# Optimization experiments

Measured on AMD Instinct MI355X. Metric: run time of the kernel, lower is better.

The kernel has to match this reference:

```python
import jax, jax.numpy as jnp
import numpy as np

F = 32  # node channels (both convs)


def ecc_conv(x, src, dst, e, fgn_w, fgn_b, root, bias):
    """Edge-conditioned conv: per-edge kernel from edge feats, gather-matmul-scatter."""
    n_nodes = x.shape[0]
    n_edges = e.shape[0]
    f_in = x.shape[1]
    # filter-generating network: (E, S) -> (E, F_in*F_out) -> (E, F_in, F_out)
    kernels = (e @ fgn_w + fgn_b).reshape(n_edges, f_in, F)
    # gather source node feats, per-edge matmul
    messages = jnp.einsum('ef,efo->eo', x[src], kernels)
    # scatter-sum to target nodes
    agg = jax.ops.segment_sum(messages, dst, num_segments=n_nodes)
    return jax.nn.relu(agg + x @ root + bias)


def setup_inputs() -> dict:
    key = jax.random.key(0)
    ks = jax.random.split(key, 12)
    N, E, S = 50000, 200000, 16
    s = 0.05  # small init scale to keep activations bounded through relu
    return {
        'x': jax.random.normal(ks[0], (N, F), jnp.float32),
        'e': jax.random.normal(ks[1], (E, S), jnp.float32),
        'src': jax.random.randint(ks[2], (E,), 0, N, jnp.int32),
        'dst': jax.random.randint(ks[3], (E,), 0, N, jnp.int32),
        'fgn_w1': jax.random.normal(ks[4], (S, F * F), jnp.float32) * s,
        'fgn_b1': jnp.zeros((F * F,), jnp.float32),
        'root1': jax.random.normal(ks[5], (F, F), jnp.float32) * s,
        'bias1': jnp.zeros((F,), jnp.float32),
        'fgn_w2': jax.random.normal(ks[6], (S, F * F), jnp.float32) * s,
        'fgn_b2': jnp.zeros((F * F,), jnp.float32),
        'root2': jax.random.normal(ks[7], (F, F), jnp.float32) * s,
        'bias2': jnp.zeros((F,), jnp.float32),
        'dense_w': jax.random.normal(ks[8], (F, 1), jnp.float32) * s,
        'dense_b': jnp.zeros((1,), jnp.float32),
    }


def reference(x, e, src, dst, fgn_w1, fgn_b1, root1, bias1,
              fgn_w2, fgn_b2, root2, bias2, dense_w, dense_b):
    h = ecc_conv(x, src, dst, e, fgn_w1, fgn_b1, root1, bias1)
    h = ecc_conv(h, src, dst, e, fgn_w2, fgn_b2, root2, bias2)
    pooled = jnp.sum(h, axis=0)          # global sum pool over nodes -> (F,)
    return pooled @ dense_w + dense_b    # (1,)
```

## Files before the change

kernel.cpp:

```cpp
#include <hip/hip_runtime.h>
#include <hip/hip_bf16.h>
#include <hip/hip_fp16.h>

#define F 32
#define S 16

typedef short v8s __attribute__((ext_vector_type(8)));
typedef _Float16 v8h __attribute__((ext_vector_type(8)));
typedef float v4f __attribute__((ext_vector_type(4)));

__device__ __forceinline__ float bf_lo(unsigned u) { return __uint_as_float(u << 16); }
__device__ __forceinline__ float bf_hi(unsigned u) { return __uint_as_float(u & 0xffff0000u); }
__device__ __forceinline__ unsigned short f2bf(float f) {
    __hip_bfloat16 h = __float2bfloat16(f);
    return *(unsigned short*)&h;
}
__device__ __forceinline__ unsigned short f2h(float f) {
    __half h = __float2half(f);
    return *(unsigned short*)&h;
}
__device__ __forceinline__ unsigned pack2(float a, float b) {
    __hip_bfloat162 h2 = __float22bfloat162_rn(make_float2(a, b));
    return *(unsigned*)&h2;
}
static inline size_t align256(size_t b) { return (b + 255) & ~(size_t)255; }

__global__ __launch_bounds__(256) void prep_kernel(
    const float* __restrict__ w1, const float* __restrict__ b1, const float* __restrict__ r1,
    const float* __restrict__ w2, const float* __restrict__ b2, const float* __restrict__ r2,
    unsigned short* __restrict__ Wf1, unsigned short* __restrict__ Wf2,
    unsigned short* __restrict__ Rt1, unsigned short* __restrict__ Rt2,
    const int* __restrict__ dst, int* __restrict__ cnt, int E)
{
    const int PER = 34 * 512 + 32 * 32;
    if (blockIdx.x < 144) {
        int tid = blockIdx.x * blockDim.x + threadIdx.x;
        if (tid >= 2 * PER) return;
        const int layer = tid / PER;
        const int rem   = tid % PER;
        const float* w = layer ? w2 : w1;
        const float* b = layer ? b2 : b1;
        const float* r = layer ? r2 : r1;
        if (rem < 34 * 512) {
            const int fi   = rem >> 9;
            const int rr   = rem & 511;
            const int lane = rr >> 3;
            const int j    = rr & 7;
            const int half = fi & 1;
            const int ck   = fi >> 1;
            const int o    = (half << 4) | (lane & 15);
            const int k    = ck * 32 + (lane >> 4) * 8 + j;
            const int s    = k >> 5, f = k & 31;
            const float v  = (s < S) ? w[s * (F * F) + f * F + o] : b[f * F + o];
            (layer ? Wf2 : Wf1)[rem] = f2h(v);
        } else {
            const int q = rem - 34 * 512;
            const int o = q >> 5, f = q & 31;
            (layer ? Rt2 : Rt1)[o * F + f] = f2bf(r[f * F + o]);
        }
    } else {
        const int e = (blockIdx.x - 144) * blockDim.x + threadIdx.x;
        if (e < E) atomicAdd(&cnt[dst[e]], 1);
    }
}

__global__ __launch_bounds__(256) void scan_partial(
    const int* __restrict__ cnt, int* __restrict__ partial, int N)
{
    const int i = blockIdx.x * 256 + threadIdx.x;
    int v = (i < N) ? cnt[i] : 0;
    #pragma unroll
    for (int off = 32; off > 0; off >>= 1) v += __shfl_down(v, off, 64);
    __shared__ int wsum[4];
    const int wave = threadIdx.x >> 6, lane = threadIdx.x & 63;
    if (lane == 0) wsum[wave] = v;
    __syncthreads();
    if (threadIdx.x == 0)
        partial[blockIdx.x] = wsum[0] + wsum[1] + wsum[2] + wsum[3];
}

__global__ void scan_top(int* __restrict__ partial, int M)
{
    const int t = threadIdx.x;
    int carry = 0;
    for (int base = 0; base < M; base += 64) {
        const int i = base + t;
        const int v0 = (i < M) ? partial[i] : 0;
        int v = v0;
        #pragma unroll
        for (int off = 1; off < 64; off <<= 1) {
            int u = __shfl_up(v, off, 64);
            if (t >= off) v += u;
        }
        if (i < M) partial[i] = carry + (v - v0);
        carry += __shfl(v, 63, 64);
    }
}

__global__ __launch_bounds__(256) void scan_final(
    const int* __restrict__ cnt, const int* __restrict__ partial,
    int* __restrict__ cursor, int* __restrict__ rowptr, int N)
{
    const int i = blockIdx.x * 256 + threadIdx.x;
    const int v0 = (i < N) ? cnt[i] : 0;
    int v = v0;
    const int wave = threadIdx.x >> 6, lane = threadIdx.x & 63;
    #pragma unroll
    for (int off = 1; off < 64; off <<= 1) {
        int u = __shfl_up(v, off, 64);
        if (lane >= off) v += u;
    }
    __shared__ int wsum[4];
    if (lane == 63) wsum[wave] = v;
    __syncthreads();
    int woff = 0;
    for (int ww = 0; ww < 4; ++ww) woff += (ww < wave) ? wsum[ww] : 0;
    if (i < N) {
        const int excl = partial[blockIdx.x] + woff + (v - v0);
        cursor[i] = excl;
        rowptr[i] = excl;
    }
}

__global__ __launch_bounds__(256) void scatter_kernel(
    const int* __restrict__ dst, int* __restrict__ cursor,
    int* __restrict__ perm, int E)
{
    int e = blockIdx.x * blockDim.x + threadIdx.x;
    if (e < E) {
        int p = atomicAdd(&cursor[dst[e]], 1);
        perm[p] = e;
    }
}

__global__ __launch_bounds__(256) void edge_msg(
    const float* __restrict__ xin,
    const float* __restrict__ ef,
    const int* __restrict__ src,
    const unsigned short* __restrict__ Wf,
    unsigned short* __restrict__ msg,
    int E)
{
    __shared__ v8h Wl[34 * 64];
    const int tid  = threadIdx.x;
    const int w    = tid >> 6;
    const int lane = tid & 63;
    const int lid  = lane & 15;
    const int quad = lane >> 4;

    {
        const uint4* s = (const uint4*)Wf;
        uint4* d = (uint4*)Wl;
        #pragma unroll
        for (int i = 0; i < 9; ++i) {
            const int idx = tid + 256 * i;
            if (idx < 2176) d[idx] = s[idx];
        }
    }
    __syncthreads();

    const int nTiles = (E + 15) >> 4;
    const int stride = gridDim.x * 4;
    int tile = blockIdx.x * 4 + w;
    if (tile >= nTiles) return;

    int  slot = tile * 16 + lid;
    bool live = (slot < E);
    int  s0   = live ? slot : 0;
    int  sn   = src[s0];
    const float4* xp = (const float4*)(xin + (size_t)sn * F + quad * 8);
    float4 xv0 = xp[0], xv1 = xp[1];
    const float4* efv = (const float4*)(ef + (size_t)s0 * S);
    float4 c0 = efv[0], c1 = efv[1], c2 = efv[2], c3 = efv[3];

    while (true) {
        const int nextTile = tile + stride;
        float4 nxv0, nxv1, nc0, nc1, nc2, nc3;
        bool nlive = false;
        if (nextTile < nTiles) {
            const int  ns_  = nextTile * 16 + lid;
            nlive = (ns_ < E);
            const int  ns0_ = nlive ? ns_ : 0;
            const int  nsn  = src[ns0_];
            const float4* nxp = (const float4*)(xin + (size_t)nsn * F + quad * 8);
            nxv0 = nxp[0]; nxv1 = nxp[1];
            const float4* nefv = (const float4*)(ef + (size_t)ns0_ * S);
            nc0 = nefv[0]; nc1 = nefv[1]; nc2 = nefv[2]; nc3 = nefv[3];
        }

        const float cs[S] = {c0.x, c0.y, c0.z, c0.w, c1.x, c1.y, c1.z, c1.w,
                             c2.x, c2.y, c2.z, c2.w, c3.x, c3.y, c3.z, c3.w};

        union { v8h h8; __half2 h2[4]; } xh;
        xh.h2[0] = __floats2half2_rn(xv0.x, xv0.y);
        xh.h2[1] = __floats2half2_rn(xv0.z, xv0.w);
        xh.h2[2] = __floats2half2_rn(xv1.x, xv1.y);
        xh.h2[3] = __floats2half2_rn(xv1.z, xv1.w);

        v4f acc0 = {0.f, 0.f, 0.f, 0.f};
        v4f acc1 = {0.f, 0.f, 0.f, 0.f};

        #pragma unroll
        for (int ck = 0; ck < S; ++ck) {
            const __half2 c2 = __floats2half2_rn(cs[ck], cs[ck]);
            union { v8h h8; __half2 h2[4]; } fr;
            fr.h2[0] = __hmul2(c2, xh.h2[0]);
            fr.h2[1] = __hmul2(c2, xh.h2[1]);
            fr.h2[2] = __hmul2(c2, xh.h2[2]);
            fr.h2[3] = __hmul2(c2, xh.h2[3]);
            acc0 = __builtin_amdgcn_mfma_f32_16x16x32_f16(Wl[(2 * ck) * 64 + lane],     fr.h8, acc0, 0, 0, 0);
            acc1 = __builtin_amdgcn_mfma_f32_16x16x32_f16(Wl[(2 * ck + 1) * 64 + lane], fr.h8, acc1, 0, 0, 0);
        }
        acc0 = __builtin_amdgcn_mfma_f32_16x16x32_f16(Wl[32 * 64 + lane], xh.h8, acc0, 0, 0, 0);
        acc1 = __builtin_amdgcn_mfma_f32_16x16x32_f16(Wl[33 * 64 + lane], xh.h8, acc1, 0, 0, 0);

        if (live) {
            unsigned short* mp = msg + (size_t)slot * 32;
            uint2 p0, p1;
            p0.x = pack2(acc0[0], acc0[1]);
            p0.y = pack2(acc0[2], acc0[3]);
            p1.x = pack2(acc1[0], acc1[1]);
            p1.y = pack2(acc1[2], acc1[3]);
            *(uint2*)(mp + quad * 4)      = p0;
            *(uint2*)(mp + 16 + quad * 4) = p1;
        }

        if (nextTile >= nTiles) break;
        tile = nextTile;
        slot = tile * 16 + lid;
        live = nlive;
        xv0 = nxv0; xv1 = nxv1;
        c0 = nc0; c1 = nc1; c2 = nc2; c3 = nc3;
    }
}

__global__ __launch_bounds__(256) void rootsum(
    const float* __restrict__ in,
    const unsigned short* __restrict__ msg,
    const int* __restrict__ rowptr,
    const int* __restrict__ cnt,
    const int* __restrict__ perm,
    const unsigned short* __restrict__ Rt,
    const float* __restrict__ bias,
    float* __restrict__ h,
    int N)
{
    __shared__ float acc[64 * 33];
    __shared__ unsigned short As[64 * F];
    const int tid  = threadIdx.x;
    const int n0   = blockIdx.x * 64;
    const int w    = tid >> 6;
    const int lane = tid & 63;
    const int lid  = lane & 15;
    const int quad = lane >> 4;

    {
        const int nl = tid >> 2;
        const int kq = tid & 3;
        int n = n0 + nl; if (n > N - 1) n = N - 1;
        const float4* xp = (const float4*)(in + (size_t)n * F + kq * 8);
        float4 v0 = xp[0], v1 = xp[1];
        uint4 pk;
        pk.x = pack2(v0.x, v0.y);
        pk.y = pack2(v0.z, v0.w);
        pk.z = pack2(v1.x, v1.y);
        pk.w = pack2(v1.z, v1.w);
        const int slot = ((nl >> 4) * 4 + kq) * 16 + (nl & 15);
        *(uint4*)(As + slot * 8) = pk;
    }

    {
        const int nl = tid >> 2;
        const int oq = tid & 3;
        const int n  = n0 + nl;
        float a[8];
        #pragma unroll
        for (int j = 0; j < 8; ++j) a[j] = 0.f;
        if (n < N) {
            const int k0 = rowptr[n];
            const int k1 = k0 + cnt[n];
            for (int k = k0; k < k1; ++k) {
                const int e = perm[k];
                const uint4 q = *(const uint4*)(msg + (size_t)e * 32 + oq * 8);
                a[0] += bf_lo(q.x); a[1] += bf_hi(q.x);
                a[2] += bf_lo(q.y); a[3] += bf_hi(q.y);
                a[4] += bf_lo(q.z); a[5] += bf_hi(q.z);
                a[6] += bf_lo(q.w); a[7] += bf_hi(q.w);
            }
        }
        float* ap = acc + nl * 33 + oq * 8;
        #pragma unroll
        for (int j = 0; j < 8; ++j) ap[j] = a[j];
    }
    __syncthreads();

    const int jt  = w & 1;
    const int ns0 = (w >> 1) * 2;
    const v8s rf = *(const v8s*)(Rt + (size_t)(jt * 16 + lid) * F + quad * 8);
    const int o0 = jt * 16 + quad * 4;
    const float4 bs = *(const float4*)(bias + o0);

    #pragma unroll
    for (int i = 0; i < 2; ++i) {
        const int ns = ns0 + i;
        const v8s af = *(const v8s*)(As + (((ns * 4 + quad) * 16) + lid) * 8);
        v4f d = {0.f, 0.f, 0.f, 0.f};
        d = __builtin_amdgcn_mfma_f32_16x16x32_bf16(rf, af, d, 0, 0, 0);
        const int n = n0 + ns * 16 + lid;
        if (n < N) {
            const float* ap = acc + (ns * 16 + lid) * 33 + o0;
            float4 hv;
            hv.x = fmaxf(d[0] + ap[0] + bs.x, 0.f);
            hv.y = fmaxf(d[1] + ap[1] + bs.y, 0.f);
            hv.z = fmaxf(d[2] + ap[2] + bs.z, 0.f);
            hv.w = fmaxf(d[3] + ap[3] + bs.w, 0.f);
            *(float4*)(h + (size_t)n * F + o0) = hv;
        }
    }
}

__global__ __launch_bounds__(256) void rootsum_pool(
    const float* __restrict__ in,
    const unsigned short* __restrict__ msg,
    const int* __restrict__ rowptr,
    const int* __restrict__ cnt,
    const int* __restrict__ perm,
    const unsigned short* __restrict__ Rt,
    const float* __restrict__ bias,
    float* __restrict__ bs,
    int N)
{
    __shared__ float acc[64 * 33];
    __shared__ unsigned short As[64 * F];
    __shared__ float poolbuf[4][16];
    const int tid  = threadIdx.x;
    const int n0   = blockIdx.x * 64;
    const int w    = tid >> 6;
    const int lane = tid & 63;
    const int lid  = lane & 15;
    const int quad = lane >> 4;

    {
        const int nl = tid >> 2;
        const int kq = tid & 3;
        int n = n0 + nl; if (n > N - 1) n = N - 1;
        const float4* xp = (const float4*)(in + (size_t)n * F + kq * 8);
        float4 v0 = xp[0], v1 = xp[1];
        uint4 pk;
        pk.x = pack2(v0.x, v0.y);
        pk.y = pack2(v0.z, v0.w);
        pk.z = pack2(v1.x, v1.y);
        pk.w = pack2(v1.z, v1.w);
        const int slot = ((nl >> 4) * 4 + kq) * 16 + (nl & 15);
        *(uint4*)(As + slot * 8) = pk;
    }

    {
        const int nl = tid >> 2;
        const int oq = tid & 3;
        const int n  = n0 + nl;
        float a[8];
        #pragma unroll
        for (int j = 0; j < 8; ++j) a[j] = 0.f;
        if (n < N) {
            const int k0 = rowptr[n];
            const int k1 = k0 + cnt[n];
            for (int k = k0; k < k1; ++k) {
                const int e = perm[k];
                const uint4 q = *(const uint4*)(msg + (size_t)e * 32 + oq * 8);
                a[0] += bf_lo(q.x); a[1] += bf_hi(q.x);
                a[2] += bf_lo(q.y); a[3] += bf_hi(q.y);
                a[4] += bf_lo(q.z); a[5] += bf_hi(q.z);
                a[6] += bf_lo(q.w); a[7] += bf_hi(q.w);
            }
        }
        float* ap = acc + nl * 33 + oq * 8;
        #pragma unroll
        for (int j = 0; j < 8; ++j) ap[j] = a[j];
    }
    __syncthreads();

    const int jt  = w & 1;
    const int ns0 = (w >> 1) * 2;
    const v8s rf = *(const v8s*)(Rt + (size_t)(jt * 16 + lid) * F + quad * 8);
    const int o0 = jt * 16 + quad * 4;
    const float4 bs4 = *(const float4*)(bias + o0);

    float psum[4] = {0.f, 0.f, 0.f, 0.f};

    #pragma unroll
    for (int i = 0; i < 2; ++i) {
        const int ns = ns0 + i;
        const v8s af = *(const v8s*)(As + (((ns * 4 + quad) * 16) + lid) * 8);
        v4f d = {0.f, 0.f, 0.f, 0.f};
        d = __builtin_amdgcn_mfma_f32_16x16x32_bf16(rf, af, d, 0, 0, 0);
        const int n = n0 + ns * 16 + lid;
        if (n < N) {
            const float* ap = acc + (ns * 16 + lid) * 33 + o0;
            psum[0] += fmaxf(d[0] + ap[0] + bs4.x, 0.f);
            psum[1] += fmaxf(d[1] + ap[1] + bs4.y, 0.f);
            psum[2] += fmaxf(d[2] + ap[2] + bs4.z, 0.f);
            psum[3] += fmaxf(d[3] + ap[3] + bs4.w, 0.f);
        }
    }

    #pragma unroll
    for (int m = 1; m < 16; m <<= 1) {
        psum[0] += __shfl_xor(psum[0], m, 64);
        psum[1] += __shfl_xor(psum[1], m, 64);
        psum[2] += __shfl_xor(psum[2], m, 64);
        psum[3] += __shfl_xor(psum[3], m, 64);
    }
    if (lid == 0) {
        #pragma unroll
        for (int j = 0; j < 4; ++j) poolbuf[w][quad * 4 + j] = psum[j];
    }
    __syncthreads();
    if (tid < 32) {
        const int jt2 = tid >> 4, idx = tid & 15;
        bs[(size_t)blockIdx.x * 32 + tid] = poolbuf[jt2][idx] + poolbuf[jt2 + 2][idx];
    }
}

__global__ __launch_bounds__(256) void final_fused(
    const float* __restrict__ bs, int nb,
    const float* __restrict__ dw, const float* __restrict__ db,
    float* __restrict__ out)
{
    const int ch = threadIdx.x & 31, g = threadIdx.x >> 5;
    float s = 0.f;
    for (int b = g; b < nb; b += 8) s += bs[(size_t)b * 32 + ch];
    __shared__ float red[256];
    red[threadIdx.x] = s;
    __syncthreads();
    if (threadIdx.x < 128) red[threadIdx.x] += red[threadIdx.x + 128];
    __syncthreads();
    if (threadIdx.x < 64) red[threadIdx.x] += red[threadIdx.x + 64];
    __syncthreads();
    if (threadIdx.x < 32) red[threadIdx.x] = (red[threadIdx.x] + red[threadIdx.x + 32]) * dw[threadIdx.x];
    __syncthreads();
    if (threadIdx.x == 0) {
        float t = 0.f;
        #pragma unroll
        for (int i = 0; i < 32; ++i) t += red[i];
        out[0] = t + db[0];
    }
}

__global__ __launch_bounds__(256) void pool_kernel(
    const float* __restrict__ h, float* __restrict__ pooled, int N)
{
    const int c = threadIdx.x & (F - 1);
    float p = 0.0f;
    for (int n = blockIdx.x * 8 + (threadIdx.x >> 5); n < N; n += gridDim.x * 8)
        p += h[(size_t)n * F + c];
    __shared__ float red[256];
    red[threadIdx.x] = p;
    __syncthreads();
    for (int off = 128; off >= F; off >>= 1) {
        if (threadIdx.x < off) red[threadIdx.x] += red[threadIdx.x + off];
        __syncthreads();
    }
    if (threadIdx.x < F) atomicAdd(&pooled[threadIdx.x], red[threadIdx.x]);
}

__global__ void final_kernel(
    const float* __restrict__ pooled, const float* __restrict__ dw,
    const float* __restrict__ db, float* __restrict__ out)
{
    const int o = threadIdx.x;
    float v = (o < F) ? pooled[o] * dw[o] : 0.0f;
    #pragma unroll
    for (int off = 32; off > 0; off >>= 1) v += __shfl_down(v, off, 64);
    if (o == 0) out[0] = v + db[0];
}

__global__ __launch_bounds__(256, 2) void ecc_edge_slow(
    const float* __restrict__ x, const float* __restrict__ ef,
    const int* __restrict__ src, const int* __restrict__ dst,
    const float* __restrict__ W, const float* __restrict__ B,
    float* __restrict__ agg, int E)
{
    const int tid = blockIdx.x * blockDim.x + threadIdx.x;
    const bool live = (tid < E);
    const int e = live ? tid : (E - 1);
    const int sn = src[e], dn = dst[e];
    float xr[F];
    const float4* xp = (const float4*)(x + (size_t)sn * F);
    #pragma unroll
    for (int i = 0; i < F / 4; ++i) {
        float4 v = xp[i];
        xr[4*i+0] = v.x; xr[4*i+1] = v.y; xr[4*i+2] = v.z; xr[4*i+3] = v.w;
    }
    float acc[F];
    #pragma unroll
    for (int o = 0; o < F; ++o) acc[o] = 0.0f;
    const float* erow = ef + (size_t)e * S;
    for (int s = 0; s < S; ++s) {
        const float es = erow[s];
        const float* Ws = W + s * (F * F);
        #pragma unroll
        for (int f = 0; f < F; ++f) {
            const float z = es * xr[f];
            #pragma unroll
            for (int o = 0; o < F; ++o) acc[o] = fmaf(z, Ws[f * F + o], acc[o]);
        }
    }
    #pragma unroll
    for (int f = 0; f < F; ++f) {
        const float xf = xr[f];
        #pragma unroll
        for (int o = 0; o < F; ++o) acc[o] = fmaf(xf, B[f * F + o], acc[o]);
    }
    if (live) {
        float* ap = agg + (size_t)dn * F;
        #pragma unroll
        for (int o = 0; o < F; ++o) atomicAdd(ap + o, acc[o]);
    }
}

__global__ __launch_bounds__(256) void ecc_node_slow(
    const float* __restrict__ xin, const float* __restrict__ root,
    const float* __restrict__ bias, float* __restrict__ h, int N)
{
    int t = blockIdx.x * blockDim.x + threadIdx.x;
    if (t >= N * F) return;
    const int n = t >> 5, o = t & (F - 1);
    const float* xrow = xin + (size_t)n * F;
    float v = h[t] + bias[o];
    #pragma unroll
    for (int f = 0; f < F; ++f) v = fmaf(xrow[f], root[f * F + o], v);
    h[t] = fmaxf(v, 0.0f);
}

extern "C" void kernel_launch(void* const* d_in, const int* in_sizes, int n_in,
                              void* d_out, int out_size, void* d_ws, size_t ws_size,
                              hipStream_t stream) {
    const float* x      = (const float*)d_in[0];
    const float* efeat  = (const float*)d_in[1];
    const int*   src    = (const int*)d_in[2];
    const int*   dst    = (const int*)d_in[3];
    const float* fgn_w1 = (const float*)d_in[4];
    const float* fgn_b1 = (const float*)d_in[5];
    const float* root1  = (const float*)d_in[6];
    const float* bias1  = (const float*)d_in[7];
    const float* fgn_w2 = (const float*)d_in[8];
    const float* fgn_b2 = (const float*)d_in[9];
    const float* root2  = (const float*)d_in[10];
    const float* bias2  = (const float*)d_in[11];
    const float* dense_w = (const float*)d_in[12];
    const float* dense_b = (const float*)d_in[13];

    const int N = in_sizes[0] / F;
    const int E = in_sizes[2];

    const int gridP    = (N + 255) / 256;
    const int rsBlocks = (N + 63) / 64;

    const size_t pooledB = 256;
    const size_t cntB    = align256((size_t)N * 4);
    const size_t rowB    = align256((size_t)N * 4);
    const size_t curB    = align256((size_t)N * 4);
    const size_t partB   = align256((size_t)gridP * 4);
    const size_t permB   = align256((size_t)E * 4);
    const size_t efsB    = align256((size_t)E * S * 4);
    const size_t srcsB   = align256((size_t)E * 4);
    const size_t msgB    = align256((size_t)E * 32 * 2);
    const size_t hB      = (size_t)N * F * 4;
    const size_t wfB     = align256((size_t)34 * 512 * 2);
    const size_t rtB     = align256((size_t)32 * 32 * 2);

    const size_t offCnt  = pooledB;
    const size_t offRow  = offCnt + cntB;
    const size_t offCur  = offRow + rowB;
    const size_t offPart = offCur + curB;
    const size_t offPerm = offPart + partB;
    const size_t offEfs  = offPerm + permB;
    const size_t offSrcs = offEfs + efsB;
    const size_t offMsg  = offSrcs + srcsB;
    const size_t offH1   = offMsg + msgB;
    const size_t offH2   = offH1 + hB;
    const size_t offW1   = offH2 + hB;
    const size_t offW2   = offW1 + wfB;
    const size_t offR1   = offW2 + wfB;
    const size_t offR2   = offR1 + rtB;
    const size_t need    = offR2 + rtB;

    const int eB         = (E + 255) / 256;
    const int nodeBlocks = (N * F + 255) / 256;

    if (ws_size >= need) {
        int* cnt     = (int*)((char*)d_ws + offCnt);
        int* rowptr  = (int*)((char*)d_ws + offRow);
        int* cursor  = (int*)((char*)d_ws + offCur);
        int* partial = (int*)((char*)d_ws + offPart);
        int* perm    = (int*)((char*)d_ws + offPerm);
        unsigned short* msg = (unsigned short*)((char*)d_ws + offMsg);
        float* h1    = (float*)((char*)d_ws + offH1);
        float* bsum  = (float*)((char*)d_ws + offH2);
        unsigned short* Wf1 = (unsigned short*)((char*)d_ws + offW1);
        unsigned short* Wf2 = (unsigned short*)((char*)d_ws + offW2);
        unsigned short* Rt1 = (unsigned short*)((char*)d_ws + offR1);
        unsigned short* Rt2 = (unsigned short*)((char*)d_ws + offR2);

        hipMemsetAsync((char*)d_ws + offCnt, 0, cntB, stream);

        prep_kernel<<<144 + eB, 256, 0, stream>>>(
            fgn_w1, fgn_b1, root1, fgn_w2, fgn_b2, root2,
            Wf1, Wf2, Rt1, Rt2, dst, cnt, E);

        scan_partial  <<<gridP, 256, 0, stream>>>(cnt, partial, N);
        scan_top      <<<1, 64, 0, stream>>>(partial, gridP);
        scan_final    <<<gridP, 256, 0, stream>>>(cnt, partial, cursor, rowptr, N);
        scatter_kernel<<<eB, 256, 0, stream>>>(dst, cursor, perm, E);

        const int nTiles = (E + 15) / 16;
        int edgeBlocks = (nTiles + 3) / 4;
        if (edgeBlocks > 1024) edgeBlocks = 1024;

        edge_msg<<<edgeBlocks, 256, 0, stream>>>(x, efeat, src, Wf1, msg, E);
        rootsum <<<rsBlocks, 256, 0, stream>>>(x, msg, rowptr, cnt, perm, Rt1, bias1, h1, N);

        edge_msg    <<<edgeBlocks, 256, 0, stream>>>(h1, efeat, src, Wf2, msg, E);
        rootsum_pool<<<rsBlocks, 256, 0, stream>>>(h1, msg, rowptr, cnt, perm, Rt2, bias2, bsum, N);

        final_fused<<<1, 256, 0, stream>>>(bsum, rsBlocks, dense_w, dense_b, (float*)d_out);
    } else {
        float* agg1   = (float*)d_ws;
        float* agg2   = agg1 + (size_t)N * F;
        float* pooled = agg2 + (size_t)N * F;
        hipMemsetAsync(d_ws, 0, (2 * (size_t)N * F + F) * sizeof(float), stream);
        ecc_edge_slow<<<eB, 256, 0, stream>>>(x, efeat, src, dst, fgn_w1, fgn_b1, agg1, E);
        ecc_node_slow<<<nodeBlocks, 256, 0, stream>>>(x, root1, bias1, agg1, N);
        ecc_edge_slow<<<eB, 256, 0, stream>>>(agg1, efeat, src, dst, fgn_w2, fgn_b2, agg2, E);
        ecc_node_slow<<<nodeBlocks, 256, 0, stream>>>(agg1, root2, bias2, agg2, N);
        pool_kernel <<<512, 256, 0, stream>>>(agg2, pooled, N);
        final_kernel<<<1, 64, 0, stream>>>(pooled, dense_w, dense_b, (float*)d_out);
    }
}
```

Baseline: 200.0 us.

## Store node features as fp16, fuse scan top-level and final reduction into neighbors

Converts the input node features to fp16 in the prep kernel and writes layer-1 output in fp16, so the edge gather and the second rootsum read half the bytes. The single-block scan_top launch is removed: each scan_final block now sums its preceding partials itself. The final pooled reduction kernel is folded into rootsum_pool with a last-block-done atomic counter. This cuts gather bandwidth and two launches, at the cost of extra fp16 rounding on the layer-1 activations and redundant partial summation in scan_final.

```diff
diff --git a/kernel.cpp b/kernel.cpp
--- a/kernel.cpp
+++ b/kernel.cpp
@@ -23,6 +23,10 @@
     __hip_bfloat162 h2 = __float22bfloat162_rn(make_float2(a, b));
     return *(unsigned*)&h2;
 }
+__device__ __forceinline__ unsigned pack2h(float a, float b) {
+    __half2 h2 = __floats2half2_rn(a, b);
+    return *(unsigned*)&h2;
+}
 static inline size_t align256(size_t b) { return (b + 255) & ~(size_t)255; }
 
 __global__ __launch_bounds__(256) void prep_kernel(
@@ -30,7 +34,9 @@
     const float* __restrict__ w2, const float* __restrict__ b2, const float* __restrict__ r2,
     unsigned short* __restrict__ Wf1, unsigned short* __restrict__ Wf2,
     unsigned short* __restrict__ Rt1, unsigned short* __restrict__ Rt2,
-    const int* __restrict__ dst, int* __restrict__ cnt, int E)
+    const int* __restrict__ dst, int* __restrict__ cnt,
+    const float* __restrict__ x, unsigned short* __restrict__ x16,
+    int N, int E, int eB)
 {
     const int PER = 34 * 512 + 32 * 32;
     if (blockIdx.x < 144) {
@@ -58,9 +64,19 @@
             const int o = q >> 5, f = q & 31;
             (layer ? Rt2 : Rt1)[o * F + f] = f2bf(r[f * F + o]);
         }
-    } else {
+    } else if (blockIdx.x < 144 + eB) {
         const int e = (blockIdx.x - 144) * blockDim.x + threadIdx.x;
         if (e < E) atomicAdd(&cnt[dst[e]], 1);
+    } else {
+        const int idx = (blockIdx.x - 144 - eB) * 256 + threadIdx.x;
+        if (idx < N * 4) {
+            const float4* p = (const float4*)(x + (size_t)idx * 8);
+            float4 a = p[0], b = p[1];
+            uint4 o;
+            o.x = pack2h(a.x, a.y); o.y = pack2h(a.z, a.w);
+            o.z = pack2h(b.x, b.y); o.w = pack2h(b.z, b.w);
+            *(uint4*)(x16 + (size_t)idx * 8) = o;
+        }
     }
 }
 
@@ -79,32 +95,27 @@
         partial[blockIdx.x] = wsum[0] + wsum[1] + wsum[2] + wsum[3];
 }
 
-__global__ void scan_top(int* __restrict__ partial, int M)
-{
-    const int t = threadIdx.x;
-    int carry = 0;
-    for (int base = 0; base < M; base += 64) {
-        const int i = base + t;
-        const int v0 = (i < M) ? partial[i] : 0;
-        int v = v0;
-        #pragma unroll
-        for (int off = 1; off < 64; off <<= 1) {
-            int u = __shfl_up(v, off, 64);
-            if (t >= off) v += u;
-        }
-        if (i < M) partial[i] = carry + (v - v0);
-        carry += __shfl(v, 63, 64);
-    }
-}
-
 __global__ __launch_bounds__(256) void scan_final(
     const int* __restrict__ cnt, const int* __restrict__ partial,
     int* __restrict__ cursor, int* __restrict__ rowptr, int N)
 {
-    const int i = blockIdx.x * 256 + threadIdx.x;
+    const int tid = threadIdx.x;
+    __shared__ int pacc[256];
+    int pre = 0;
+    for (int j = tid; j < blockIdx.x; j += 256) pre += partial[j];
+    pacc[tid] = pre;
+    __syncthreads();
+    #pragma unroll
+    for (int off = 128; off > 0; off >>= 1) {
+        if (tid < off) pacc[tid] += pacc[tid + off];
+        __syncthreads();
+    }
+    const int blockPre = pacc[0];
+
+    const int i = blockIdx.x * 256 + tid;
     const int v0 = (i < N) ? cnt[i] : 0;
     int v = v0;
-    const int wave = threadIdx.x >> 6, lane = threadIdx.x & 63;
+    const int wave = tid >> 6, lane = tid & 63;
     #pragma unroll
     for (int off = 1; off < 64; off <<= 1) {
         int u = __shfl_up(v, off, 64);
@@ -116,7 +127,7 @@
     int woff = 0;
     for (int ww = 0; ww < 4; ++ww) woff += (ww < wave) ? wsum[ww] : 0;
     if (i < N) {
-        const int excl = partial[blockIdx.x] + woff + (v - v0);
+        const int excl = blockPre + woff + (v - v0);
         cursor[i] = excl;
         rowptr[i] = excl;
     }
@@ -134,7 +145,7 @@
 }
 
 __global__ __launch_bounds__(256) void edge_msg(
-    const float* __restrict__ xin,
+    const unsigned short* __restrict__ x16,
     const float* __restrict__ ef,
     const int* __restrict__ src,
     const unsigned short* __restrict__ Wf,
@@ -168,22 +179,21 @@
     bool live = (slot < E);
     int  s0   = live ? slot : 0;
     int  sn   = src[s0];
-    const float4* xp = (const float4*)(xin + (size_t)sn * F + quad * 8);
-    float4 xv0 = xp[0], xv1 = xp[1];
+    v8h xh = *(const v8h*)(x16 + (size_t)sn * F + quad * 8);
     const float4* efv = (const float4*)(ef + (size_t)s0 * S);
     float4 c0 = efv[0], c1 = efv[1], c2 = efv[2], c3 = efv[3];
 
     while (true) {
         const int nextTile = tile + stride;
-        float4 nxv0, nxv1, nc0, nc1, nc2, nc3;
+        v8h nxh;
+        float4 nc0, nc1, nc2, nc3;
         bool nlive = false;
         if (nextTile < nTiles) {
             const int  ns_  = nextTile * 16 + lid;
             nlive = (ns_ < E);
             const int  ns0_ = nlive ? ns_ : 0;
             const int  nsn  = src[ns0_];
-            const float4* nxp = (const float4*)(xin + (size_t)nsn * F + quad * 8);
-            nxv0 = nxp[0]; nxv1 = nxp[1];
+            nxh = *(const v8h*)(x16 + (size_t)nsn * F + quad * 8);
             const float4* nefv = (const float4*)(ef + (size_t)ns0_ * S);
             nc0 = nefv[0]; nc1 = nefv[1]; nc2 = nefv[2]; nc3 = nefv[3];
         }
@@ -191,28 +201,25 @@
         const float cs[S] = {c0.x, c0.y, c0.z, c0.w, c1.x, c1.y, c1.z, c1.w,
                              c2.x, c2.y, c2.z, c2.w, c3.x, c3.y, c3.z, c3.w};
 
-        union { v8h h8; __half2 h2[4]; } xh;
-        xh.h2[0] = __floats2half2_rn(xv0.x, xv0.y);
-        xh.h2[1] = __floats2half2_rn(xv0.z, xv0.w);
-        xh.h2[2] = __floats2half2_rn(xv1.x, xv1.y);
-        xh.h2[3] = __floats2half2_rn(xv1.z, xv1.w);
+        union { v8h h8; __half2 h2[4]; } xu;
+        xu.h8 = xh;
 
         v4f acc0 = {0.f, 0.f, 0.f, 0.f};
         v4f acc1 = {0.f, 0.f, 0.f, 0.f};
 
         #pragma unroll
         for (int ck = 0; ck < S; ++ck) {
-            const __half2 c2 = __floats2half2_rn(cs[ck], cs[ck]);
+            const __half2 cc = __floats2half2_rn(cs[ck], cs[ck]);
             union { v8h h8; __half2 h2[4]; } fr;
-            fr.h2[0] = __hmul2(c2, xh.h2[0]);
-            fr.h2[1] = __hmul2(c2, xh.h2[1]);
-            fr.h2[2] = __hmul2(c2, xh.h2[2]);
-            fr.h2[3] = __hmul2(c2, xh.h2[3]);
+            fr.h2[0] = __hmul2(cc, xu.h2[0]);
+            fr.h2[1] = __hmul2(cc, xu.h2[1]);
+            fr.h2[2] = __hmul2(cc, xu.h2[2]);
+            fr.h2[3] = __hmul2(cc, xu.h2[3]);
             acc0 = __builtin_amdgcn_mfma_f32_16x16x32_f16(Wl[(2 * ck) * 64 + lane],     fr.h8, acc0, 0, 0, 0);
             acc1 = __builtin_amdgcn_mfma_f32_16x16x32_f16(Wl[(2 * ck + 1) * 64 + lane], fr.h8, acc1, 0, 0, 0);
         }
-        acc0 = __builtin_amdgcn_mfma_f32_16x16x32_f16(Wl[32 * 64 + lane], xh.h8, acc0, 0, 0, 0);
-        acc1 = __builtin_amdgcn_mfma_f32_16x16x32_f16(Wl[33 * 64 + lane], xh.h8, acc1, 0, 0, 0);
+        acc0 = __builtin_amdgcn_mfma_f32_16x16x32_f16(Wl[32 * 64 + lane], xu.h8, acc0, 0, 0, 0);
+        acc1 = __builtin_amdgcn_mfma_f32_16x16x32_f16(Wl[33 * 64 + lane], xu.h8, acc1, 0, 0, 0);
 
         if (live) {
             unsigned short* mp = msg + (size_t)slot * 32;
@@ -229,7 +236,7 @@
         tile = nextTile;
         slot = tile * 16 + lid;
         live = nlive;
-        xv0 = nxv0; xv1 = nxv1;
+        xh = nxh;
         c0 = nc0; c1 = nc1; c2 = nc2; c3 = nc3;
     }
 }
@@ -242,7 +249,7 @@
     const int* __restrict__ perm,
     const unsigned short* __restrict__ Rt,
     const float* __restrict__ bias,
-    float* __restrict__ h,
+    unsigned short* __restrict__ h16,
     int N)
 {
     __shared__ float acc[64 * 33];
@@ -314,13 +321,16 @@
             hv.y = fmaxf(d[1] + ap[1] + bs.y, 0.f);
             hv.z = fmaxf(d[2] + ap[2] + bs.z, 0.f);
             hv.w = fmaxf(d[3] + ap[3] + bs.w, 0.f);
-            *(float4*)(h + (size_t)n * F + o0) = hv;
+            uint2 hp;
+            hp.x = pack2h(hv.x, hv.y);
+            hp.y = pack2h(hv.z, hv.w);
+            *(uint2*)(h16 + (size_t)n * F + o0) = hp;
         }
     }
 }
 
 __global__ __launch_bounds__(256) void rootsum_pool(
-    const float* __restrict__ in,
+    const unsigned short* __restrict__ in16,
     const unsigned short* __restrict__ msg,
     const int* __restrict__ rowptr,
     const int* __restrict__ cnt,
@@ -328,6 +338,10 @@
     const unsigned short* __restrict__ Rt,
     const float* __restrict__ bias,
     float* __restrict__ bs,
+    int* __restrict__ flag,
+    const float* __restrict__ dw,
+    const float* __restrict__ db,
+    float* __restrict__ out,
     int N)
 {
     __shared__ float acc[64 * 33];
@@ -344,13 +358,17 @@
         const int nl = tid >> 2;
         const int kq = tid & 3;
         int n = n0 + nl; if (n > N - 1) n = N - 1;
-        const float4* xp = (const float4*)(in + (size_t)n * F + kq * 8);
-        float4 v0 = xp[0], v1 = xp[1];
+        const uint4 hv4 = *(const uint4*)(in16 + (size_t)n * F + kq * 8);
+        const __half2* hh = (const __half2*)&hv4;
+        float2 f0 = __half22float2(hh[0]);
+        float2 f1 = __half22float2(hh[1]);
+        float2 f2 = __half22float2(hh[2]);
+        float2 f3 = __half22float2(hh[3]);
         uint4 pk;
-        pk.x = pack2(v0.x, v0.y);
-        pk.y = pack2(v0.z, v0.w);
-        pk.z = pack2(v1.x, v1.y);
-        pk.w = pack2(v1.z, v1.w);
+        pk.x = pack2(f0.x, f0.y);
+        pk.y = pack2(f1.x, f1.y);
+        pk.z = pack2(f2.x, f2.y);
+        pk.w = pack2(f3.x, f3.y);
         const int slot = ((nl >> 4) * 4 + kq) * 16 + (nl & 15);
         *(uint4*)(As + slot * 8) = pk;
     }
@@ -420,30 +438,35 @@
         const int jt2 = tid >> 4, idx = tid & 15;
         bs[(size_t)blockIdx.x * 32 + tid] = poolbuf[jt2][idx] + poolbuf[jt2 + 2][idx];
     }
-}
-
-__global__ __launch_bounds__(256) void final_fused(
-    const float* __restrict__ bs, int nb,
-    const float* __restrict__ dw, const float* __restrict__ db,
-    float* __restrict__ out)
-{
-    const int ch = threadIdx.x & 31, g = threadIdx.x >> 5;
-    float s = 0.f;
-    for (int b = g; b < nb; b += 8) s += bs[(size_t)b * 32 + ch];
-    __shared__ float red[256];
-    red[threadIdx.x] = s;
-    __syncthreads();
-    if (threadIdx.x < 128) red[threadIdx.x] += red[threadIdx.x + 128];
-    __syncthreads();
-    if (threadIdx.x < 64) red[threadIdx.x] += red[threadIdx.x + 64];
-    __syncthreads();
-    if (threadIdx.x < 32) red[threadIdx.x] = (red[threadIdx.x] + red[threadIdx.x + 32]) * dw[threadIdx.x];
-    __syncthreads();
-    if (threadIdx.x == 0) {
-        float t = 0.f;
-        #pragma unroll
-        for (int i = 0; i < 32; ++i) t += red[i];
-        out[0] = t + db[0];
+
+    __shared__ int amLast;
+    __threadfence();
+    if (tid == 0) {
+        const int prev = atomicAdd(flag, 1);
+        amLast = (prev == (int)gridDim.x - 1);
+    }
+    __syncthreads();
+    if (amLast) {
+        __threadfence();
+        const int ch = tid & 31, g = tid >> 5;
+        float s = 0.f;
+        const int nb = gridDim.x;
+        for (int b = g; b < nb; b += 8) s += bs[(size_t)b * 32 + ch];
+        __shared__ float red[256];
+        red[tid] = s;
+        __syncthreads();
+        if (tid < 128) red[tid] += red[tid + 128];
+        __syncthreads();
+        if (tid < 64) red[tid] += red[tid + 64];
+        __syncthreads();
+        if (tid < 32) red[tid] = (red[tid] + red[tid + 32]) * dw[tid];
+        __syncthreads();
+        if (tid == 0) {
+            float t = 0.f;
+            #pragma unroll
+            for (int i = 0; i < 32; ++i) t += red[i];
+            out[0] = t + db[0];
+        }
     }
 }
 
@@ -569,6 +592,7 @@
     const size_t hB      = (size_t)N * F * 4;
     const size_t wfB     = align256((size_t)34 * 512 * 2);
     const size_t rtB     = align256((size_t)32 * 32 * 2);
+    const size_t x16B    = align256((size_t)N * F * 2);
 
     const size_t offCnt  = pooledB;
     const size_t offRow  = offCnt + cntB;
@@ -589,28 +613,30 @@
     const int eB         = (E + 255) / 256;
     const int nodeBlocks = (N * F + 255) / 256;
 
-    if (ws_size >= need) {
+    if (ws_size >= need && efsB >= 2 * x16B) {
+        int* flag    = (int*)d_ws;
         int* cnt     = (int*)((char*)d_ws + offCnt);
         int* rowptr  = (int*)((char*)d_ws + offRow);
         int* cursor  = (int*)((char*)d_ws + offCur);
         int* partial = (int*)((char*)d_ws + offPart);
         int* perm    = (int*)((char*)d_ws + offPerm);
+        unsigned short* x16 = (unsigned short*)((char*)d_ws + offEfs);
+        unsigned short* h16 = (unsigned short*)((char*)d_ws + offEfs + x16B);
         unsigned short* msg = (unsigned short*)((char*)d_ws + offMsg);
-        float* h1    = (float*)((char*)d_ws + offH1);
         float* bsum  = (float*)((char*)d_ws + offH2);
         unsigned short* Wf1 = (unsigned short*)((char*)d_ws + offW1);
         unsigned short* Wf2 = (unsigned short*)((char*)d_ws + offW2);
         unsigned short* Rt1 = (unsigned short*)((char*)d_ws + offR1);
         unsigned short* Rt2 = (unsigned short*)((char*)d_ws + offR2);
 
-        hipMemsetAsync((char*)d_ws + offCnt, 0, cntB, stream);
-
-        prep_kernel<<<144 + eB, 256, 0, stream>>>(
+        hipMemsetAsync(d_ws, 0, pooledB + cntB, stream);
+
+        const int xcB = (N * 4 + 255) / 256;
+        prep_kernel<<<144 + eB + xcB, 256, 0, stream>>>(
             fgn_w1, fgn_b1, root1, fgn_w2, fgn_b2, root2,
-            Wf1, Wf2, Rt1, Rt2, dst, cnt, E);
+            Wf1, Wf2, Rt1, Rt2, dst, cnt, x, x16, N, E, eB);
 
         scan_partial  <<<gridP, 256, 0, stream>>>(cnt, partial, N);
-        scan_top      <<<1, 64, 0, stream>>>(partial, gridP);
         scan_final    <<<gridP, 256, 0, stream>>>(cnt, partial, cursor, rowptr, N);
         scatter_kernel<<<eB, 256, 0, stream>>>(dst, cursor, perm, E);
 
@@ -618,13 +644,13 @@
         int edgeBlocks = (nTiles + 3) / 4;
         if (edgeBlocks > 1024) edgeBlocks = 1024;
 
-        edge_msg<<<edgeBlocks, 256, 0, stream>>>(x, efeat, src, Wf1, msg, E);
-        rootsum <<<rsBlocks, 256, 0, stream>>>(x, msg, rowptr, cnt, perm, Rt1, bias1, h1, N);
-
-        edge_msg    <<<edgeBlocks, 256, 0, stream>>>(h1, efeat, src, Wf2, msg, E);
-        rootsum_pool<<<rsBlocks, 256, 0, stream>>>(h1, msg, rowptr, cnt, perm, Rt2, bias2, bsum, N);
-
-        final_fused<<<1, 256, 0, stream>>>(bsum, rsBlocks, dense_w, dense_b, (float*)d_out);
+        edge_msg<<<edgeBlocks, 256, 0, stream>>>(x16, efeat, src, Wf1, msg, E);
+        rootsum <<<rsBlocks, 256, 0, stream>>>(x, msg, rowptr, cnt, perm, Rt1, bias1, h16, N);
+
+        edge_msg    <<<edgeBlocks, 256, 0, stream>>>(h16, efeat, src, Wf2, msg, E);
+        rootsum_pool<<<rsBlocks, 256, 0, stream>>>(h16, msg, rowptr, cnt, perm, Rt2, bias2,
+                                                   bsum, flag, dense_w, dense_b,
+                                                   (float*)d_out, N);
     } else {
         float* agg1   = (float*)d_ws;
         float* agg2   = agg1 + (size_t)N * F;
```

Measured after the change: 238.8 us. 19.4% more time.
